# Optimization experiments

Measured on AMD Instinct MI355X. Metric: run time of the kernel, lower is better.

The kernel has to match this reference:

```python
import jax, jax.numpy as jnp
import numpy as np

B, N, F_IN = 8, 1024, 25   # batch, num_edges (GAT nodes), features_per_link = 1 + 8*num_bands
H, D = 8, 16               # num_heads, output_dim per head (hidden_size // num_heads)
NEG_INF = -9e15            # matches torch -9000000000000000.0


def setup_inputs() -> dict:
    key = jax.random.key(0)
    k1, k2, k3, k4 = jax.random.split(key, 4)
    node_feats = jax.random.normal(k1, (B, N, F_IN), dtype=jnp.float32)
    adj = jax.random.randint(k2, (B, N, N), 0, 2, dtype=jnp.int32)
    # Xavier-uniform-ish params per GATLayer.reset_parameters (gain for relu)
    gain = float(np.sqrt(2.0))
    limW = gain * np.sqrt(6.0 / (F_IN + D))
    lima = gain * np.sqrt(6.0 / (2 * D + 1))
    W = jax.random.uniform(k3, (H, F_IN, D), jnp.float32, -limW, limW)
    a = jax.random.uniform(k4, (H, 2 * D, 1), jnp.float32, -lima, lima)
    return {"node_feats": node_feats, "adj": adj, "W": W, "a": a}


def reference(node_feats, adj, W, a):
    d = W.shape[-1]
    # Wh: [B, H, N, D]
    Wh = jnp.einsum('bnf,hfd->bhnd', node_feats, W)
    # Additive attention: e_ij = <Wh_i, a_src> + <Wh_j, a_dst>  (no LeakyReLU in this module)
    a_src = a[:, :d, 0]   # [H, D]
    a_dst = a[:, d:, 0]   # [H, D]
    ei = jnp.einsum('bhnd,hd->bhn', Wh, a_src)  # [B, H, N]
    ej = jnp.einsum('bhnd,hd->bhn', Wh, a_dst)  # [B, H, N]
    e = ei[:, :, :, None] + ej[:, :, None, :]   # [B, H, N, N]
    mask = adj[:, None, :, :].astype(bool)      # [B, 1->H, N, N]
    e = jnp.where(mask, e, jnp.asarray(NEG_INF, e.dtype))
    alpha = jax.nn.softmax(e, axis=-1)          # dropout is identity at eval
    h_prime = jnp.einsum('bhij,bhjd->bhid', alpha, Wh)        # [B, H, N, D]
    h_prime = h_prime.transpose(0, 2, 1, 3).reshape(node_feats.shape[0], node_feats.shape[1], -1)
    return jax.nn.relu(h_prime), alpha
```

## Files before the change

kernel.cpp:

```cpp
#include <hip/hip_runtime.h>

#define L2E 1.44269504f

typedef short short8_t  __attribute__((ext_vector_type(8)));
typedef float fltx4     __attribute__((ext_vector_type(4)));
typedef int   intx4     __attribute__((ext_vector_type(4)));
typedef unsigned short ushort4_t __attribute__((ext_vector_type(4)));
typedef unsigned int uint32;

__device__ __forceinline__ unsigned short f2bf(float f) {
    uint32 u = __float_as_uint(f);
    u += 0x7FFFu + ((u >> 16) & 1u);
    return (unsigned short)(u >> 16);
}

__global__ __launch_bounds__(256) void prep_once(
    const float* __restrict__ x,
    const float* __restrict__ W,
    const float* __restrict__ a,
    float* __restrict__ pexp_ws,
    unsigned short* __restrict__ whb)
{
    int t  = blockIdx.x * 256 + threadIdx.x;
    int bh = t >> 10, n = t & 1023;
    int b  = bh >> 3, h = bh & 7;

    const float* xr = x + ((size_t)(b * 1024 + n)) * 25;
    const float* Wp = W + h * 400;
    const float* ap = a + h * 32;

    float xf[25];
    #pragma unroll
    for (int f = 0; f < 25; ++f) xf[f] = xr[f];

    int base = ((bh * 32 + (n >> 5)) * 64 + ((n >> 3) & 3) * 16) * 8 + (n & 7);
    float vj = 0.f;
    #pragma unroll
    for (int d = 0; d < 16; ++d) {
        float s = 0.f;
        #pragma unroll
        for (int f = 0; f < 25; ++f) s += xf[f] * Wp[f * 16 + d];
        vj += s * ap[16 + d];
        whb[base + d * 8] = f2bf(s);
    }
    pexp_ws[t] = exp2f(vj * L2E);
}

__global__ __launch_bounds__(256) void gat_main(
    const int*   __restrict__ adj,
    const float* __restrict__ pexp_ws,
    const unsigned short* __restrict__ whb,
    float* __restrict__ out0,
    float* __restrict__ out1)
{
    __shared__ __align__(16) unsigned short tlds[4][4][1024];

    const int blk   = blockIdx.x;
    const int b     = blk >> 6;
    const int chunk = blk & 63;
    const int wave  = threadIdx.x >> 6;
    const int lane  = threadIdx.x & 63;
    const int i0    = chunk * 16 + wave * 4;
    const int mrow  = lane & 15;
    const int quad  = lane >> 4;

    const intx4* adjb = (const intx4*)(adj + ((size_t)b * 1024 + i0) * 1024);
    uint32 msk[4];
    #pragma unroll
    for (int r = 0; r < 4; ++r) {
        uint32 m = 0;
        #pragma unroll
        for (int j0 = 0; j0 < 4; ++j0) {
            intx4 a4 = adjb[r * 256 + j0 * 64 + lane];
            m |= (a4.x ? (1u << (j0 * 4 + 0)) : 0u);
            m |= (a4.y ? (1u << (j0 * 4 + 1)) : 0u);
            m |= (a4.z ? (1u << (j0 * 4 + 2)) : 0u);
            m |= (a4.w ? (1u << (j0 * 4 + 3)) : 0u);
        }
        msk[r] = m;
    }

    char* tl = (char*)&tlds[wave][0][0];

    for (int h = 0; h < 8; ++h) {
        const int bh = b * 8 + h;

        const fltx4* pe4 = (const fltx4*)(pexp_ws + bh * 1024);
        fltx4 ev[4];
        #pragma unroll
        for (int j0 = 0; j0 < 4; ++j0) ev[j0] = pe4[j0 * 64 + lane];

        float sum[4];
        #pragma unroll
        for (int r = 0; r < 4; ++r) {
            float s0 = 0.f;
            const uint32 m = msk[r];
            #pragma unroll
            for (int j0 = 0; j0 < 4; ++j0) {
                s0 += ((m >> (j0 * 4 + 0)) & 1u) ? ev[j0].x : 0.f;
                s0 += ((m >> (j0 * 4 + 1)) & 1u) ? ev[j0].y : 0.f;
                s0 += ((m >> (j0 * 4 + 2)) & 1u) ? ev[j0].z : 0.f;
                s0 += ((m >> (j0 * 4 + 3)) & 1u) ? ev[j0].w : 0.f;
            }
            sum[r] = s0;
        }
        #pragma unroll
        for (int off = 32; off; off >>= 1) {
            #pragma unroll
            for (int r = 0; r < 4; ++r) sum[r] += __shfl_xor(sum[r], off);
        }

        float* abase = out1 + (size_t)bh * 1024 * 1024;
        #pragma unroll
        for (int r = 0; r < 4; ++r) {
            const bool ok = sum[r] > 0.f;
            const float rinv = ok ? __builtin_amdgcn_rcpf(sum[r]) : 0.f;
            const float fbv  = ok ? 0.f : (1.0f / 1024.0f);
            const uint32 m = msk[r];
            const int swz = r << 6;
            #pragma unroll
            for (int j0 = 0; j0 < 4; ++j0) {
                fltx4 st;
                st.x = ((m >> (j0 * 4 + 0)) & 1u) ? ev[j0].x * rinv + fbv : fbv;
                st.y = ((m >> (j0 * 4 + 1)) & 1u) ? ev[j0].y * rinv + fbv : fbv;
                st.z = ((m >> (j0 * 4 + 2)) & 1u) ? ev[j0].z * rinv + fbv : fbv;
                st.w = ((m >> (j0 * 4 + 3)) & 1u) ? ev[j0].w * rinv + fbv : fbv;
                __builtin_nontemporal_store(st,
                    (fltx4*)(abase + (size_t)(i0 + r) * 1024 + j0 * 256 + lane * 4));
                ushort4_t bv;
                bv.x = f2bf(st.x); bv.y = f2bf(st.y);
                bv.z = f2bf(st.z); bv.w = f2bf(st.w);
                *(ushort4_t*)(tl + r * 2048 + ((j0 * 512 + lane * 8) ^ swz)) = bv;
            }
        }

        const unsigned short* bbase = whb + (size_t)bh * 16384;
        const int arow = mrow & 3;
        const int aswz = arow << 6;
        fltx4 acc = {0.f, 0.f, 0.f, 0.f};
        #pragma unroll 8
        for (int ks = 0; ks < 32; ++ks) {
            short8_t afr = *(const short8_t*)(tl + arow * 2048 +
                             ((ks * 64 + quad * 16) ^ aswz));
            short8_t bfr = *(const short8_t*)(bbase + ((ks * 64 + lane) << 3));
            acc = __builtin_amdgcn_mfma_f32_16x16x32_bf16(afr, bfr, acc, 0, 0, 0);
        }
        if (quad == 0) {
            #pragma unroll
            for (int r = 0; r < 4; ++r) {
                float v = acc[r] > 0.f ? acc[r] : 0.f;
                out0[((size_t)(b * 1024 + i0 + r)) * 128 + h * 16 + mrow] = v;
            }
        }
    }
}

__global__ __launch_bounds__(256) void gat_fused(
    const float* __restrict__ x, const int* __restrict__ adj,
    const float* __restrict__ W, const float* __restrict__ a,
    float* __restrict__ out0, float* __restrict__ out1)
{
    __shared__ __align__(16) unsigned short whb[32 * 64 * 8];
    __shared__ __align__(16) float ej_lds[1024];
    __shared__ float ei_lds[64];
    __shared__ float wa[64];

    const int bh    = blockIdx.x >> 4;
    const int chunk = blockIdx.x & 15;
    const int b     = bh >> 3;
    const int h     = bh & 7;
    const int tid   = threadIdx.x;
    const int wave  = tid >> 6;
    const int lane  = tid & 63;
    const int mrow  = lane & 15;
    const int quad  = lane >> 4;

    const float* Wp = W + h * 400;
    const float* ap = a + h * 32;
    const float* xb = x + (size_t)b * 1024 * 25;

    if (tid < 50) {
        int f = tid % 25, which = tid / 25;
        float s = 0.f;
        #pragma unroll
        for (int d = 0; d < 16; ++d) s += Wp[f * 16 + d] * ap[which * 16 + d];
        wa[which * 32 + f] = s;
    }
    __syncthreads();

    for (int s = 0; s < 4; ++s) {
        int n = tid + (s << 8);
        const float* xr = xb + n * 25;
        float xf[25];
        #pragma unroll
        for (int f = 0; f < 25; ++f) xf[f] = xr[f];
        float vi = 0.f, vj = 0.f;
        #pragma unroll
        for (int f = 0; f < 25; ++f) { vi += xf[f] * wa[f]; vj += xf[f] * wa[32 + f]; }
        ej_lds[n] = vj;
        if ((n >> 6) == chunk) ei_lds[n & 63] = vi;
        int base = (((n >> 5) * 64 + ((n >> 3) & 3) * 16) << 3) + (n & 7);
        #pragma unroll
        for (int d = 0; d < 16; ++d) {
            float s2 = 0.f;
            #pragma unroll
            for (int f = 0; f < 25; ++f) s2 += xf[f] * Wp[f * 16 + d];
            whb[base + d * 8] = f2bf(s2);
        }
    }
    __syncthreads();

    const int i0 = chunk * 64 + wave * 16;
    float* abase = out1 + (size_t)bh * 1024 * 1024;
    const fltx4* ej4 = (const fltx4*)ej_lds;

    for (int r = 0; r < 16; ++r) {
        int i = i0 + r;
        float s_ei = ei_lds[wave * 16 + r];
        const intx4* adj4 = (const intx4*)(adj + ((size_t)b * 1024 + i) * 1024);
        float p[16];
        float sum = 0.f;
        #pragma unroll
        for (int j0 = 0; j0 < 4; ++j0) {
            intx4 av = adj4[j0 * 64 + lane];
            fltx4 ev = ej4[j0 * 64 + lane];
            float p0 = av.x ? exp2f((s_ei + ev.x) * L2E) : 0.f;
            float p1 = av.y ? exp2f((s_ei + ev.y) * L2E) : 0.f;
            float p2 = av.z ? exp2f((s_ei + ev.z) * L2E) : 0.f;
            float p3 = av.w ? exp2f((s_ei + ev.w) * L2E) : 0.f;
            p[j0 * 4 + 0] = p0; p[j0 * 4 + 1] = p1;
            p[j0 * 4 + 2] = p2; p[j0 * 4 + 3] = p3;
            sum += (p0 + p1) + (p2 + p3);
        }
        #pragma unroll
        for (int off = 32; off; off >>= 1) sum += __shfl_xor(sum, off);
        float rinv;
        if (sum > 0.f) {
            rinv = __builtin_amdgcn_rcpf(sum);
        } else {
            rinv = 1.0f;
            #pragma unroll
            for (int k = 0; k < 16; ++k) p[k] = 1.0f / 1024.0f;
        }
        float* arow = abase + (size_t)i * 1024;
        #pragma unroll
        for (int j0 = 0; j0 < 4; ++j0) {
            fltx4 st;
            st.x = p[j0 * 4 + 0] * rinv; st.y = p[j0 * 4 + 1] * rinv;
            st.z = p[j0 * 4 + 2] * rinv; st.w = p[j0 * 4 + 3] * rinv;
            *(fltx4*)(arow + (j0 * 64 + lane) * 4) = st;
        }
    }

    __builtin_amdgcn_fence(__ATOMIC_ACQ_REL, "workgroup");

    const float* aptr = abase + (size_t)(i0 + mrow) * 1024 + quad * 8;
    fltx4 acc = {0.f, 0.f, 0.f, 0.f};
    for (int ks = 0; ks < 32; ++ks) {
        fltx4 a0 = *(const fltx4*)(aptr + ks * 32);
        fltx4 a1 = *(const fltx4*)(aptr + ks * 32 + 4);
        short8_t afr;
        #pragma unroll
        for (int q = 0; q < 4; ++q) {
            afr[q]     = (short)f2bf(a0[q]);
            afr[4 + q] = (short)f2bf(a1[q]);
        }
        short8_t bfr = *(const short8_t*)&whb[((ks * 64 + lane) << 3)];
        acc = __builtin_amdgcn_mfma_f32_16x16x32_bf16(afr, bfr, acc, 0, 0, 0);
    }
    #pragma unroll
    for (int r = 0; r < 4; ++r) {
        int i = i0 + quad * 4 + r;
        float v = acc[r] > 0.f ? acc[r] : 0.f;
        out0[((size_t)(b * 1024 + i)) * 128 + h * 16 + mrow] = v;
    }
}

extern "C" void kernel_launch(void* const* d_in, const int* in_sizes, int n_in,
                              void* d_out, int out_size, void* d_ws, size_t ws_size,
                              hipStream_t stream) {
    const float* x   = (const float*)d_in[0];
    const int*   adj = (const int*)d_in[1];
    const float* W   = (const float*)d_in[2];
    const float* a   = (const float*)d_in[3];

    float* out0 = (float*)d_out;
    float* out1 = out0 + (size_t)8 * 1024 * 128;

    const size_t WHB_BYTES = (size_t)64 * 16384 * 2;
    const size_t EJ_BYTES  = (size_t)64 * 1024 * 4;
    const size_t NEED      = WHB_BYTES + EJ_BYTES;

    if (ws_size >= NEED) {
        unsigned short* whb = (unsigned short*)d_ws;
        float* pexp_ws = (float*)((char*)d_ws + WHB_BYTES);
        prep_once<<<256, 256, 0, stream>>>(x, W, a, pexp_ws, whb);
        gat_main<<<512, 256, 0, stream>>>(adj, pexp_ws, whb, out0, out1);
    } else {
        gat_fused<<<1024, 256, 0, stream>>>(x, adj, W, a, out0, out1);
    }
}
```

Before: 302.5 us.

## Share block-wide attention tile in LDS and split MFMA K across waves

Previously each wave ran its own 32-step MFMA over a 4-row tile padded into a 16-row fragment, so three quarters of the MFMA rows were wasted. Now the four waves write a shared 16-row bf16 alpha tile. Each wave handles 8 of the 32 K-steps on all 16 rows, and partial sums are reduced through LDS before wave 0 writes out0. The next head's exp values are also prefetched while the current head is processed. This costs two __syncthreads per head, an extra LDS reduction, and holding the prefetched values in registers.

```diff
diff --git a/kernel.cpp b/kernel.cpp
--- a/kernel.cpp
+++ b/kernel.cpp
@@ -53,18 +53,20 @@
     float* __restrict__ out0,
     float* __restrict__ out1)
 {
-    __shared__ __align__(16) unsigned short tlds[4][4][1024];
+    __shared__ __align__(16) unsigned short atile[16][1024];
+    __shared__ __align__(16) float accred[4][16][16];
 
     const int blk   = blockIdx.x;
     const int b     = blk >> 6;
     const int chunk = blk & 63;
     const int wave  = threadIdx.x >> 6;
     const int lane  = threadIdx.x & 63;
-    const int i0    = chunk * 16 + wave * 4;
+    const int i0c   = chunk * 16;
+    const int i0w   = i0c + wave * 4;
     const int mrow  = lane & 15;
     const int quad  = lane >> 4;
 
-    const intx4* adjb = (const intx4*)(adj + ((size_t)b * 1024 + i0) * 1024);
+    const intx4* adjb = (const intx4*)(adj + ((size_t)b * 1024 + i0w) * 1024);
     uint32 msk[4];
     #pragma unroll
     for (int r = 0; r < 4; ++r) {
@@ -80,15 +82,15 @@
         msk[r] = m;
     }
 
-    char* tl = (char*)&tlds[wave][0][0];
+    char* tlb = (char*)&atile[0][0];
+
+    const fltx4* pe4 = (const fltx4*)(pexp_ws + (size_t)(b * 8) * 1024);
+    fltx4 ev[4];
+    #pragma unroll
+    for (int j0 = 0; j0 < 4; ++j0) ev[j0] = pe4[j0 * 64 + lane];
 
     for (int h = 0; h < 8; ++h) {
         const int bh = b * 8 + h;
-
-        const fltx4* pe4 = (const fltx4*)(pexp_ws + bh * 1024);
-        fltx4 ev[4];
-        #pragma unroll
-        for (int j0 = 0; j0 < 4; ++j0) ev[j0] = pe4[j0 * 64 + lane];
 
         float sum[4];
         #pragma unroll
@@ -110,6 +112,13 @@
             for (int r = 0; r < 4; ++r) sum[r] += __shfl_xor(sum[r], off);
         }
 
+        fltx4 evn[4];
+        if (h < 7) {
+            const fltx4* pn = (const fltx4*)(pexp_ws + (size_t)(bh + 1) * 1024);
+            #pragma unroll
+            for (int j0 = 0; j0 < 4; ++j0) evn[j0] = pn[j0 * 64 + lane];
+        }
+
         float* abase = out1 + (size_t)bh * 1024 * 1024;
         #pragma unroll
         for (int r = 0; r < 4; ++r) {
@@ -117,7 +126,9 @@
             const float rinv = ok ? __builtin_amdgcn_rcpf(sum[r]) : 0.f;
             const float fbv  = ok ? 0.f : (1.0f / 1024.0f);
             const uint32 m = msk[r];
-            const int swz = r << 6;
+            const int row  = wave * 4 + r;
+            const int swz  = (row & 7) << 4;
+            char* lrow = tlb + row * 2048;
             #pragma unroll
             for (int j0 = 0; j0 < 4; ++j0) {
                 fltx4 st;
@@ -126,32 +137,48 @@
                 st.z = ((m >> (j0 * 4 + 2)) & 1u) ? ev[j0].z * rinv + fbv : fbv;
                 st.w = ((m >> (j0 * 4 + 3)) & 1u) ? ev[j0].w * rinv + fbv : fbv;
                 __builtin_nontemporal_store(st,
-                    (fltx4*)(abase + (size_t)(i0 + r) * 1024 + j0 * 256 + lane * 4));
+                    (fltx4*)(abase + (size_t)(i0w + r) * 1024 + j0 * 256 + lane * 4));
                 ushort4_t bv;
                 bv.x = f2bf(st.x); bv.y = f2bf(st.y);
                 bv.z = f2bf(st.z); bv.w = f2bf(st.w);
-                *(ushort4_t*)(tl + r * 2048 + ((j0 * 512 + lane * 8) ^ swz)) = bv;
+                *(ushort4_t*)(lrow + ((j0 * 512 + lane * 8) ^ swz)) = bv;
             }
         }
 
-        const unsigned short* bbase = whb + (size_t)bh * 16384;
-        const int arow = mrow & 3;
-        const int aswz = arow << 6;
-        fltx4 acc = {0.f, 0.f, 0.f, 0.f};
-        #pragma unroll 8
-        for (int ks = 0; ks < 32; ++ks) {
-            short8_t afr = *(const short8_t*)(tl + arow * 2048 +
-                             ((ks * 64 + quad * 16) ^ aswz));
-            short8_t bfr = *(const short8_t*)(bbase + ((ks * 64 + lane) << 3));
-            acc = __builtin_amdgcn_mfma_f32_16x16x32_bf16(afr, bfr, acc, 0, 0, 0);
-        }
-        if (quad == 0) {
+        __syncthreads();
+
+        {
+            const unsigned short* bbase = whb + (size_t)bh * 16384;
+            const int aswz = (mrow & 7) << 4;
+            char* lrow = tlb + mrow * 2048;
+            fltx4 acc = {0.f, 0.f, 0.f, 0.f};
+            #pragma unroll
+            for (int kk = 0; kk < 8; ++kk) {
+                const int ks = wave * 8 + kk;
+                short8_t afr = *(const short8_t*)(lrow + ((ks * 64 + quad * 16) ^ aswz));
+                short8_t bfr = *(const short8_t*)(bbase + ((ks * 64 + lane) << 3));
+                acc = __builtin_amdgcn_mfma_f32_16x16x32_bf16(afr, bfr, acc, 0, 0, 0);
+            }
+            #pragma unroll
+            for (int r = 0; r < 4; ++r)
+                accred[wave][quad * 4 + r][mrow] = acc[r];
+        }
+
+        __syncthreads();
+
+        if (wave == 0) {
             #pragma unroll
             for (int r = 0; r < 4; ++r) {
-                float v = acc[r] > 0.f ? acc[r] : 0.f;
-                out0[((size_t)(b * 1024 + i0 + r)) * 128 + h * 16 + mrow] = v;
+                const int row = quad * 4 + r;
+                float v = (accred[0][row][mrow] + accred[1][row][mrow])
+                        + (accred[2][row][mrow] + accred[3][row][mrow]);
+                v = v > 0.f ? v : 0.f;
+                out0[((size_t)(b * 1024 + i0c + row)) * 128 + h * 16 + mrow] = v;
             }
         }
+
+        #pragma unroll
+        for (int j0 = 0; j0 < 4; ++j0) ev[j0] = evn[j0];
     }
 }
 
```

After: 298.3 us (median of 2 runs). No clear change (-1.4%).
